# Kernel tuning notes

Hardware: AMD Instinct MI355X
Metric: run time of the kernel (lower is better)

Reference implementation:

```python
import jax, jax.numpy as jnp
import numpy as np
import math

N = 4096
E = 512          # hidden_dim
H = 8            # num_heads
MAX_STEPS = 100
D_TIME = E // 2  # 256
D_STAT = E // 4  # 128


def _time_encoding():
    # sinusoidal table [MAX_STEPS, D_TIME], matching the torch buffer
    pos = jnp.arange(MAX_STEPS, dtype=jnp.float32)[:, None]
    div = jnp.exp(jnp.arange(0, D_TIME, 2, dtype=jnp.float32) * (-math.log(10000.0) / D_TIME))
    ang = pos * div  # [MAX_STEPS, D_TIME//2]
    return jnp.stack([jnp.sin(ang), jnp.cos(ang)], axis=-1).reshape(MAX_STEPS, D_TIME)


def setup_inputs() -> dict:
    key = jax.random.key(0)
    ks = jax.random.split(key, 12)
    w = 0.02
    return {
        "x": jax.random.normal(ks[0], (N, E), jnp.float32),
        "derived_mask": jax.random.randint(ks[1], (N,), 0, 2, jnp.int32),
        "step_numbers": jax.random.randint(ks[2], (N,), 0, MAX_STEPS, jnp.int32),
        "status_embed": jax.random.normal(ks[3], (2, D_STAT), jnp.float32),
        "in_proj_w": jax.random.normal(ks[4], (3 * E, E), jnp.float32) * w,
        "in_proj_b": jnp.zeros((3 * E,), jnp.float32),
        "out_proj_w": jax.random.normal(ks[5], (E, E), jnp.float32) * w,
        "out_proj_b": jnp.zeros((E,), jnp.float32),
        "mlp_w": jax.random.normal(ks[6], (E, E + D_STAT + D_TIME), jnp.float32) * w,
        "mlp_b": jnp.zeros((E,), jnp.float32),
        "ln_gamma": jnp.ones((E,), jnp.float32),
        "ln_beta": jnp.zeros((E,), jnp.float32),
    }


def reference(x, derived_mask, step_numbers, status_embed, in_proj_w, in_proj_b,
              out_proj_w, out_proj_b, mlp_w, mlp_b, ln_gamma, ln_beta):
    n = x.shape[0]
    hd = E // H

    # --- multihead self-attention with dynamic step-based mask ---
    qkv = x @ in_proj_w.T + in_proj_b                      # [N, 3E]
    q, k, v = jnp.split(qkv, 3, axis=-1)
    q = q.reshape(n, H, hd).transpose(1, 0, 2)             # [H, N, hd]
    k = k.reshape(n, H, hd).transpose(1, 0, 2)
    v = v.reshape(n, H, hd).transpose(1, 0, 2)

    scores = jnp.einsum('hnd,hmd->hnm', q, k) / math.sqrt(hd)   # [H, N, N]
    # mask[i, j] = True  <=>  step[j] - step[i] < 0 (blocked, -inf)
    blocked = (step_numbers[None, :] - step_numbers[:, None]) < 0
    scores = jnp.where(blocked[None, :, :], jnp.float32(-1e9), scores)
    attn = jax.nn.softmax(scores, axis=-1)
    ctx = jnp.einsum('hnm,hmd->hnd', attn, v)              # [H, N, hd]
    ctx = ctx.transpose(1, 0, 2).reshape(n, E)
    x_att = ctx @ out_proj_w.T + out_proj_b                # [N, E]

    # --- embeddings ---
    status = status_embed[derived_mask]                    # [N, E/4]
    step_c = jnp.clip(step_numbers, 0, MAX_STEPS - 1)
    time_emb = _time_encoding()[step_c]                    # [N, E/2]

    # --- fused output MLP: Linear -> LayerNorm -> ReLU ---
    combined = jnp.concatenate([x_att, status, time_emb], axis=-1)  # [N, 7E/4]
    h = combined @ mlp_w.T + mlp_b                         # [N, E]
    mu = jnp.mean(h, axis=-1, keepdims=True)
    var = jnp.mean((h - mu) ** 2, axis=-1, keepdims=True)
    h = (h - mu) / jnp.sqrt(var + 1e-5) * ln_gamma + ln_beta
    out = jnp.maximum(h, 0.0)
    return x + out
```

## Files before the change

### kernel.cpp

```cpp
#include <hip/hip_runtime.h>
#include <hip/hip_bf16.h>
#include <math.h>

typedef __bf16 bf16x8 __attribute__((ext_vector_type(8)));
typedef __bf16 bf16x4 __attribute__((ext_vector_type(4)));
typedef float f32x4 __attribute__((ext_vector_type(4)));
typedef float f32x16 __attribute__((ext_vector_type(16)));

#define N_TOK 4096
#define EDIM 512
#define NHEAD 8
#define HD 64
#define LDCOMB 896
#define NBIN 100
#define SPLITK 4
#define BK 64
#define NQT 32

#define NU_CVT 3264
#define NU_TC 64
#define NU_ADD 128
#define NU_TMAT 128
#define NB_PREP (NU_CVT + NU_TC + NU_ADD + NU_TMAT + 1)

__device__ __forceinline__ unsigned int pk2(float a, float b) {
    union { __bf16 h[2]; unsigned int u; } x;
    x.h[0] = (__bf16)a; x.h[1] = (__bf16)b;
    return x.u;
}

__global__ __launch_bounds__(256) void prep_kernel(
    const float* __restrict__ x, const float* __restrict__ w_in,
    const float* __restrict__ w_mlp, const float* __restrict__ w_out,
    const float* __restrict__ status, const float* __restrict__ out_b,
    const float* __restrict__ mlp_b, const int* __restrict__ steps,
    __bf16* __restrict__ x_bf, __bf16* __restrict__ wqkv_bf,
    __bf16* __restrict__ wmlp_bf, __bf16* __restrict__ woutT_bf,
    float* __restrict__ add2, __bf16* __restrict__ tmat,
    int* __restrict__ perm, int* __restrict__ sstep,
    int* __restrict__ bs_row, int* __restrict__ qinfo) {
    __shared__ float T[64][65];
    __shared__ int hist[NBIN];
    __shared__ int offs[NBIN];
    const int bid = blockIdx.x;
    const int tid = threadIdx.x;
    const int wave = tid >> 6, lane = tid & 63;

    if (bid < NU_CVT) {
        int i = bid * 256 + tid;
        const int n0 = N_TOK * EDIM / 4;
        const int n1 = 3 * EDIM * EDIM / 4;
        const float* src; __bf16* dst;
        if (i < n0)           { src = x; dst = x_bf; }
        else if (i < n0 + n1) { i -= n0; src = w_in; dst = wqkv_bf; }
        else                  { i -= n0 + n1; src = w_mlp; dst = wmlp_bf; }
        const float4 v = ((const float4*)src)[i];
        bf16x4 o;
        o[0] = (__bf16)v.x; o[1] = (__bf16)v.y; o[2] = (__bf16)v.z; o[3] = (__bf16)v.w;
        ((bf16x4*)dst)[i] = o;
    } else if (bid < NU_CVT + NU_TC) {
        const int b2 = bid - NU_CVT;
        const int m0 = (b2 >> 3) * 64, k0 = (b2 & 7) * 64;
        const int row = tid >> 2, c4 = (tid & 3) * 16;
        #pragma unroll
        for (int i = 0; i < 4; i++) {
            const float4 v = *(const float4*)&w_out[(size_t)(m0 + row) * EDIM + k0 + c4 + i * 4];
            T[row][c4 + i * 4 + 0] = v.x;
            T[row][c4 + i * 4 + 1] = v.y;
            T[row][c4 + i * 4 + 2] = v.z;
            T[row][c4 + i * 4 + 3] = v.w;
        }
        __syncthreads();
        const int kr = tid >> 2, m16 = (tid & 3) * 16;
        bf16x8 o0, o1;
        #pragma unroll
        for (int i = 0; i < 8; i++) o0[i] = (__bf16)T[m16 + i][kr];
        #pragma unroll
        for (int i = 0; i < 8; i++) o1[i] = (__bf16)T[m16 + 8 + i][kr];
        *(bf16x8*)&woutT_bf[(size_t)(k0 + kr) * EDIM + m0 + m16] = o0;
        *(bf16x8*)&woutT_bf[(size_t)(k0 + kr) * EDIM + m0 + m16 + 8] = o1;
    } else if (bid < NU_CVT + NU_TC + NU_ADD) {
        const int j = (bid - NU_CVT - NU_TC) * 4 + wave;
        const float* wr = w_mlp + (size_t)j * LDCOMB;
        const int k8 = lane * 8;
        const float4 wa = *(const float4*)&wr[k8], wb = *(const float4*)&wr[k8 + 4];
        const float4 oa = *(const float4*)&out_b[k8], ob = *(const float4*)&out_b[k8 + 4];
        float b = wa.x * oa.x + wa.y * oa.y + wa.z * oa.z + wa.w * oa.w +
                  wb.x * ob.x + wb.y * ob.y + wb.z * ob.z + wb.w * ob.w;
        const int c2 = lane * 2;
        const float w0 = wr[EDIM + c2], w1 = wr[EDIM + c2 + 1];
        float s0 = status[c2] * w0 + status[c2 + 1] * w1;
        float s1 = status[128 + c2] * w0 + status[129 + c2] * w1;
        #pragma unroll
        for (int m = 1; m < 64; m <<= 1) {
            b += __shfl_xor(b, m);
            s0 += __shfl_xor(s0, m);
            s1 += __shfl_xor(s1, m);
        }
        if (lane == 0) {
            const float bb = b + mlp_b[j];
            add2[j] = s0 + bb;
            add2[EDIM + j] = s1 + bb;
        }
    } else if (bid < NU_CVT + NU_TC + NU_ADD + NU_TMAT) {
        const int st = bid - NU_CVT - NU_TC - NU_ADD;
        const int c = tid;
        const int pp = c >> 1;
        const float div = expf((float)(2 * pp) * (-9.210340371976184f / 256.0f));
        const float ang = (float)st * div;
        tmat[st * 256 + c] = (__bf16)((c & 1) ? cosf(ang) : sinf(ang));
    } else {
        if (tid < NBIN) hist[tid] = 0;
        __syncthreads();
        for (int i = tid; i < N_TOK; i += 256)
            atomicAdd(&hist[min(max(steps[i], 0), NBIN - 1)], 1);
        __syncthreads();
        if (tid == 0) {
            int acc = 0;
            for (int s = 0; s < NBIN; s++) { offs[s] = acc; acc += hist[s]; }
        }
        __syncthreads();
        if (tid < NBIN) hist[tid] = offs[tid];
        __syncthreads();
        for (int i = tid; i < N_TOK; i += 256) {
            const int s = min(max(steps[i], 0), NBIN - 1);
            const int pos = atomicAdd(&offs[s], 1);
            perm[pos] = i;
            sstep[pos] = s;
        }
        __syncthreads();
        for (int q = tid; q < N_TOK; q += 256)
            bs_row[q] = hist[sstep[q]];
        __syncthreads();
        for (int qt = tid; qt < NQT; qt += 256) {
            qinfo[qt * 2] = bs_row[qt * 128] & ~(BK - 1);
            qinfo[qt * 2 + 1] = bs_row[qt * 128 + 127];
        }
    }
}

__global__ __launch_bounds__(256) void gemm2_kernel(const __bf16* __restrict__ x_bf,
                                                    const __bf16* __restrict__ wqkv_bf,
                                                    const float* __restrict__ b_in,
                                                    const int* __restrict__ perm,
                                                    __bf16* __restrict__ qs,
                                                    __bf16* __restrict__ ks,
                                                    __bf16* __restrict__ vt,
                                                    const __bf16* __restrict__ wmlp_bf,
                                                    const __bf16* __restrict__ woutT_bf,
                                                    __bf16* __restrict__ weff_bf,
                                                    const __bf16* __restrict__ tmat,
                                                    float* __restrict__ tv) {
    __shared__ __attribute__((aligned(16))) union {
        struct { __bf16 As[128][40]; __bf16 Bs[128][40]; } g;
        __bf16 T[128][72];
    } sm;
    __shared__ int pr[128];
    const int bid = blockIdx.x;
    const int tid = threadIdx.x;
    const int wave = tid >> 6, lane = tid & 63;
    const int wm = (wave >> 1) * 64, wn = (wave & 1) * 64;
    const int lr = lane & 15, lq = lane >> 4;

    const __bf16 *A, *B;
    int lda, ldb, bm, bn, K, mode;
    if (bid < 384) {
        A = x_bf; lda = EDIM; B = wqkv_bf; ldb = EDIM; K = EDIM; mode = 0;
        bm = (bid & 31) * 128; bn = (bid >> 5) * 128;
        if (tid < 128) pr[tid] = perm[bm + tid];
    } else if (bid < 400) {
        const int b2 = bid - 384;
        A = wmlp_bf; lda = LDCOMB; B = woutT_bf; ldb = EDIM; K = EDIM; mode = 1;
        bm = (b2 & 3) * 128; bn = (b2 >> 2) * 128;
    } else {
        const int b3 = bid - 400;
        A = tmat; lda = 256; B = wmlp_bf + 640; ldb = LDCOMB; K = 256; mode = 2;
        bm = 0; bn = b3 * 128;
    }

    f32x4 acc[4][4] = {};
    for (int k0 = 0; k0 < K; k0 += 32) {
        __syncthreads();
        #pragma unroll
        for (int c = tid; c < 512; c += 256) {
            const int row = c >> 2, k8 = (c & 3) * 8;
            const int arow = (mode == 0) ? pr[row] : (bm + row);
            *(bf16x8*)&sm.g.As[row][k8] = *(const bf16x8*)&A[(size_t)arow * lda + k0 + k8];
            *(bf16x8*)&sm.g.Bs[row][k8] = *(const bf16x8*)&B[(size_t)(bn + row) * ldb + k0 + k8];
        }
        __syncthreads();
        bf16x8 af[4], bfr[4];
        #pragma unroll
        for (int i = 0; i < 4; i++) {
            af[i]  = *(const bf16x8*)&sm.g.As[wm + i * 16 + lr][lq * 8];
            bfr[i] = *(const bf16x8*)&sm.g.Bs[wn + i * 16 + lr][lq * 8];
        }
        #pragma unroll
        for (int i = 0; i < 4; i++)
            #pragma unroll
            for (int j = 0; j < 4; j++)
                acc[i][j] = __builtin_amdgcn_mfma_f32_16x16x32_bf16(af[i], bfr[j], acc[i][j], 0, 0, 0);
    }

    if (mode == 1) {
        #pragma unroll
        for (int i = 0; i < 4; i++)
            #pragma unroll
            for (int j = 0; j < 4; j++) {
                const int col = bn + wn + j * 16 + lr;
                #pragma unroll
                for (int r = 0; r < 4; r++)
                    weff_bf[(size_t)(bm + wm + i * 16 + lq * 4 + r) * EDIM + col] =
                        (__bf16)acc[i][j][r];
            }
    } else if (mode == 2) {
        #pragma unroll
        for (int i = 0; i < 4; i++)
            #pragma unroll
            for (int j = 0; j < 4; j++) {
                const int col = bn + wn + j * 16 + lr;
                #pragma unroll
                for (int r = 0; r < 4; r++) {
                    const int row = wm + i * 16 + lq * 4 + r;
                    if (row < NBIN) tv[(size_t)row * EDIM + col] = acc[i][j][r];
                }
            }
    } else if (bn < 512) {
        const float SC = 0.125f * 1.44269504f;
        #pragma unroll
        for (int i = 0; i < 4; i++)
            #pragma unroll
            for (int j = 0; j < 4; j++) {
                const int col = bn + wn + j * 16 + lr;
                const float bv = b_in[col];
                #pragma unroll
                for (int r = 0; r < 4; r++)
                    qs[(size_t)(bm + wm + i * 16 + lq * 4 + r) * EDIM + col] =
                        (__bf16)((acc[i][j][r] + bv) * SC);
            }
    } else if (bn < 1024) {
        #pragma unroll
        for (int i = 0; i < 4; i++)
            #pragma unroll
            for (int j = 0; j < 4; j++) {
                const int col = bn + wn + j * 16 + lr;
                const float bv = b_in[col];
                #pragma unroll
                for (int r = 0; r < 4; r++)
                    ks[(size_t)(bm + wm + i * 16 + lq * 4 + r) * EDIM + (col - 512)] =
                        (__bf16)(acc[i][j][r] + bv);
            }
    } else {
        #pragma unroll
        for (int half = 0; half < 2; half++) {
            __syncthreads();
            if ((wave & 1) == half) {
                #pragma unroll
                for (int i = 0; i < 4; i++)
                    #pragma unroll
                    for (int j = 0; j < 4; j++) {
                        const float bv = b_in[bn + wn + j * 16 + lr];
                        #pragma unroll
                        for (int r = 0; r < 4; r++)
                            sm.T[wm + i * 16 + lq * 4 + r][j * 16 + lr] =
                                (__bf16)(acc[i][j][r] + bv);
                    }
            }
            __syncthreads();
            for (int u = tid; u < 1024; u += 256) {
                const int d = u & 63, t8 = (u >> 6) * 8;
                bf16x8 v;
                #pragma unroll
                for (int j = 0; j < 8; j++) v[j] = sm.T[t8 + j][d];
                const int dim = (bn - 1024) + half * 64 + d;
                *(bf16x8*)&vt[(size_t)dim * N_TOK + bm + t8] = v;
            }
        }
    }
}

__global__ __launch_bounds__(256, 4) void attn_kernel(const __bf16* __restrict__ qs,
                                                      const __bf16* __restrict__ ks,
                                                      const __bf16* __restrict__ vt,
                                                      const int* __restrict__ bs_row,
                                                      const int* __restrict__ qinfo,
                                                      __bf16* __restrict__ po,
                                                      float* __restrict__ pl) {
    __shared__ __attribute__((aligned(16))) __bf16 KVs[2][2][4160];

    const int h = blockIdx.x & 7;
    const int qtile = blockIdx.x >> 3;
    const int ck = blockIdx.y;
    const int tid = threadIdx.x, wave = tid >> 6, lane = tid & 63;
    const int l31 = lane & 31, hi = lane >> 5;
    const int wq0 = qtile * 128 + wave * 32;

    const int kt0 = qinfo[qtile * 2];
    const int bs_blockmax = qinfo[qtile * 2 + 1];
    const int nt = (N_TOK - kt0) / BK;
    const int kta = kt0 + ((nt * ck) / SPLITK) * BK;
    const int ktb = kt0 + ((nt * (ck + 1)) / SPLITK) * BK;

    bf16x8 aq[4];
    {
        const __bf16* qrow = qs + (size_t)(wq0 + l31) * EDIM + h * HD;
        #pragma unroll
        for (int m = 0; m < 4; m++) aq[m] = *(const bf16x8*)&qrow[m * 16 + hi * 8];
    }
    const int bsq = bs_row[wq0 + l31];

    bf16x8 ones;
    #pragma unroll
    for (int i = 0; i < 8; i++) ones[i] = (__bf16)1.0f;

    f32x16 lacc = {};
    f32x16 o0 = {}, o1 = {};

    const int ro = lane >> 3;
    const int sc = (lane & 7) ^ ro;

    auto stage = [&](int buf, int kt_s) {
        #pragma unroll
        for (int i = 0; i < 2; i++) {
            const int g = wave * 2 + i;
            const __bf16* gk = ks + (size_t)(kt_s + g * 8 + ro) * EDIM + h * HD + sc * 8;
            __builtin_amdgcn_global_load_lds(
                (const __attribute__((address_space(1))) unsigned int*)gk,
                (__attribute__((address_space(3))) unsigned int*)&KVs[buf][0][g * 520],
                16, 0, 0);
            const __bf16* gv = vt + (size_t)(h * HD + g * 8 + ro) * N_TOK + kt_s + sc * 8;
            __builtin_amdgcn_global_load_lds(
                (const __attribute__((address_space(1))) unsigned int*)gv,
                (__attribute__((address_space(3))) unsigned int*)&KVs[buf][1][g * 520],
                16, 0, 0);
        }
    };

    #define LDOFF(r, c) (((r) >> 3) * 520 + ((r) & 7) * 64 + ((((c) ^ ((r) & 7))) << 3))

    if (kta < ktb) stage(0, kta);
    __syncthreads();

    int cur = 0;
    for (int kt = kta; kt < ktb; kt += BK) {
        if (kt + BK < ktb) stage(cur ^ 1, kt + BK);
        const __bf16* Kl = &KVs[cur][0][0];
        const __bf16* Vl = &KVs[cur][1][0];

        __builtin_amdgcn_s_setprio(1);
        #pragma unroll
        for (int t = 0; t < 2; t++) {
            f32x16 s = {};
            #pragma unroll
            for (int m = 0; m < 4; m++) {
                const bf16x8 kb = *(const bf16x8*)&Kl[LDOFF(t * 32 + l31, 2 * m + hi)];
                s = __builtin_amdgcn_mfma_f32_32x32x16_bf16(kb, aq[m], s, 0, 0, 0);
            }
            if (kt < bs_blockmax) {
                const int tokb = kt + t * 32 + 4 * hi;
                #pragma unroll
                for (int r = 0; r < 16; r++) {
                    const int tok = tokb + (r & 3) + 8 * (r >> 2);
                    if (tok < bsq) s[r] = -1e9f;
                }
            }
            unsigned int pk[8];
            #pragma unroll
            for (int m = 0; m < 8; m++)
                pk[m] = pk2(exp2f(s[2 * m]), exp2f(s[2 * m + 1]));
            asm("v_permlane32_swap_b32 %0, %1" : "+v"(pk[0]), "+v"(pk[2]));
            asm("v_permlane32_swap_b32 %0, %1" : "+v"(pk[1]), "+v"(pk[3]));
            asm("v_permlane32_swap_b32 %0, %1" : "+v"(pk[4]), "+v"(pk[6]));
            asm("v_permlane32_swap_b32 %0, %1" : "+v"(pk[5]), "+v"(pk[7]));
            union { unsigned int u[4]; bf16x8 v; } f0, f1;
            f0.u[0] = pk[0]; f0.u[1] = pk[1]; f0.u[2] = pk[2]; f0.u[3] = pk[3];
            f1.u[0] = pk[4]; f1.u[1] = pk[5]; f1.u[2] = pk[6]; f1.u[3] = pk[7];
            lacc = __builtin_amdgcn_mfma_f32_32x32x16_bf16(ones, f0.v, lacc, 0, 0, 0);
            lacc = __builtin_amdgcn_mfma_f32_32x32x16_bf16(ones, f1.v, lacc, 0, 0, 0);
            #pragma unroll
            for (int h2 = 0; h2 < 2; h2++) {
                const bf16x8 va = *(const bf16x8*)&Vl[LDOFF(l31, 4 * t + 2 * h2 + hi)];
                const bf16x8 vb = *(const bf16x8*)&Vl[LDOFF(32 + l31, 4 * t + 2 * h2 + hi)];
                const bf16x8 pf = h2 ? f1.v : f0.v;
                o0 = __builtin_amdgcn_mfma_f32_32x32x16_bf16(va, pf, o0, 0, 0, 0);
                o1 = __builtin_amdgcn_mfma_f32_32x32x16_bf16(vb, pf, o1, 0, 0, 0);
            }
        }
        __builtin_amdgcn_s_setprio(0);
        __syncthreads();
        cur ^= 1;
    }
    #undef LDOFF

    __bf16* pob = po + (((size_t)(ck * NHEAD + h) * N_TOK) + wq0 + l31) * HD;
    #pragma unroll
    for (int rg = 0; rg < 4; rg++) {
        bf16x4 ova, ovb;
        #pragma unroll
        for (int r = 0; r < 4; r++) { ova[r] = (__bf16)o0[rg * 4 + r]; ovb[r] = (__bf16)o1[rg * 4 + r]; }
        *(bf16x4*)&pob[rg * 8 + 4 * hi] = ova;
        *(bf16x4*)&pob[32 + rg * 8 + 4 * hi] = ovb;
    }
    if (hi == 0)
        pl[(size_t)(ck * NHEAD + h) * N_TOK + wq0 + l31] = lacc[0];
}

__global__ __launch_bounds__(256) void combine_kernel(const __bf16* __restrict__ po,
                                                      const float* __restrict__ pl,
                                                      const int* __restrict__ perm,
                                                      __bf16* __restrict__ ctx) {
    const int e = blockIdx.x * 256 + threadIdx.x;
    const int q = e >> 7;
    const int col = (e & 127) * 4;
    const int h = col >> 6, d = col & 63;
    float s0 = 0.f, s1 = 0.f, s2 = 0.f, s3 = 0.f, l = 0.f;
    #pragma unroll
    for (int c = 0; c < SPLITK; c++) {
        const bf16x4 v = *(const bf16x4*)&po[(((size_t)(c * NHEAD + h) * N_TOK) + q) * HD + d];
        s0 += (float)v[0]; s1 += (float)v[1]; s2 += (float)v[2]; s3 += (float)v[3];
        l += pl[(size_t)(c * NHEAD + h) * N_TOK + q];
    }
    const float rl = 1.0f / l;
    bf16x4 o;
    o[0] = (__bf16)(s0 * rl); o[1] = (__bf16)(s1 * rl);
    o[2] = (__bf16)(s2 * rl); o[3] = (__bf16)(s3 * rl);
    *(bf16x4*)&ctx[(size_t)perm[q] * EDIM + col] = o;
}

__global__ __launch_bounds__(256) void gemm_fused(const __bf16* __restrict__ A,
                                                  const __bf16* __restrict__ B,
                                                  const int* __restrict__ dmask,
                                                  const int* __restrict__ steps,
                                                  const float* __restrict__ add2,
                                                  const float* __restrict__ tv,
                                                  float* __restrict__ C) {
    __shared__ __attribute__((aligned(16))) __bf16 As[128][40];
    __shared__ __attribute__((aligned(16))) __bf16 Bs[128][40];
    const int tid = threadIdx.x;
    const int wave = tid >> 6, lane = tid & 63;
    const int wm = (wave >> 1) * 64, wn = (wave & 1) * 64;
    const int bm = blockIdx.x * 128, bn = blockIdx.y * 128;
    const int lr = lane & 15, lq = lane >> 4;

    f32x4 acc[4][4] = {};
    for (int k0 = 0; k0 < EDIM; k0 += 32) {
        __syncthreads();
        #pragma unroll
        for (int c = tid; c < 512; c += 256) {
            const int row = c >> 2, k8 = (c & 3) * 8;
            *(bf16x8*)&As[row][k8] = *(const bf16x8*)&A[(size_t)(bm + row) * EDIM + k0 + k8];
            *(bf16x8*)&Bs[row][k8] = *(const bf16x8*)&B[(size_t)(bn + row) * EDIM + k0 + k8];
        }
        __syncthreads();
        bf16x8 af[4], bfr[4];
        #pragma unroll
        for (int i = 0; i < 4; i++) {
            af[i]  = *(const bf16x8*)&As[wm + i * 16 + lr][lq * 8];
            bfr[i] = *(const bf16x8*)&Bs[wn + i * 16 + lr][lq * 8];
        }
        #pragma unroll
        for (int i = 0; i < 4; i++)
            #pragma unroll
            for (int j = 0; j < 4; j++)
                acc[i][j] = __builtin_amdgcn_mfma_f32_16x16x32_bf16(af[i], bfr[j], acc[i][j], 0, 0, 0);
    }

    int dmr[4][4], str[4][4];
    #pragma unroll
    for (int i = 0; i < 4; i++)
        #pragma unroll
        for (int r = 0; r < 4; r++) {
            const int row = bm + wm + i * 16 + lq * 4 + r;
            dmr[i][r] = dmask[row];
            str[i][r] = min(max(steps[row], 0), NBIN - 1);
        }
    #pragma unroll
    for (int i = 0; i < 4; i++)
        #pragma unroll
        for (int j = 0; j < 4; j++) {
            const int col = bn + wn + j * 16 + lr;
            #pragma unroll
            for (int r = 0; r < 4; r++) {
                const int row = bm + wm + i * 16 + lq * 4 + r;
                C[(size_t)row * EDIM + col] = acc[i][j][r]
                    + add2[dmr[i][r] * EDIM + col] + tv[str[i][r] * EDIM + col];
            }
        }
}

__global__ __launch_bounds__(256) void ln_kernel(const float* __restrict__ h,
                                                 const float* __restrict__ x,
                                                 const float* __restrict__ gamma,
                                                 const float* __restrict__ beta,
                                                 float* __restrict__ out) {
    const int row = blockIdx.x * 4 + (threadIdx.x >> 6);
    const int lane = threadIdx.x & 63;
    const float* hr = h + (size_t)row * EDIM;
    float4 v0 = ((const float4*)hr)[lane];
    float4 v1 = ((const float4*)hr)[64 + lane];
    float sum = v0.x + v0.y + v0.z + v0.w + v1.x + v1.y + v1.z + v1.w;
    float sq = v0.x * v0.x + v0.y * v0.y + v0.z * v0.z + v0.w * v0.w +
               v1.x * v1.x + v1.y * v1.y + v1.z * v1.z + v1.w * v1.w;
    #pragma unroll
    for (int m = 1; m < 64; m <<= 1) {
        sum += __shfl_xor(sum, m);
        sq  += __shfl_xor(sq, m);
    }
    const float mean = sum * (1.0f / EDIM);
    const float var = sq * (1.0f / EDIM) - mean * mean;
    const float rstd = rsqrtf(var + 1e-5f);
    const float* xr = x + (size_t)row * EDIM;
    float* orow = out + (size_t)row * EDIM;
    #pragma unroll
    for (int half = 0; half < 2; half++) {
        const float4 v = half ? v1 : v0;
        const int cb = half * 256 + lane * 4;
        const float* vp = (const float*)&v;
        float4 res;
        float tmp[4];
        #pragma unroll
        for (int i = 0; i < 4; i++) {
            const int c = cb + i;
            float t = (vp[i] - mean) * rstd * gamma[c] + beta[c];
            t = fmaxf(t, 0.f);
            tmp[i] = xr[c] + t;
        }
        res.x = tmp[0]; res.y = tmp[1]; res.z = tmp[2]; res.w = tmp[3];
        ((float4*)orow)[cb >> 2] = res;
    }
}

extern "C" void kernel_launch(void* const* d_in, const int* in_sizes, int n_in,
                              void* d_out, int out_size, void* d_ws, size_t ws_size,
                              hipStream_t stream) {
    const float* x      = (const float*)d_in[0];
    const int*   dmask  = (const int*)d_in[1];
    const int*   steps  = (const int*)d_in[2];
    const float* status = (const float*)d_in[3];
    const float* w_in   = (const float*)d_in[4];
    const float* b_in   = (const float*)d_in[5];
    const float* w_out  = (const float*)d_in[6];
    const float* b_out  = (const float*)d_in[7];
    const float* w_mlp  = (const float*)d_in[8];
    const float* b_mlp  = (const float*)d_in[9];
    const float* gamma  = (const float*)d_in[10];
    const float* beta   = (const float*)d_in[11];
    float* out = (float*)d_out;

    char* ws = (char*)d_ws;
    size_t off = 0;
    auto alloc = [&](size_t bytes) {
        void* ptr = ws + off;
        off = (off + bytes + 255) & ~(size_t)255;
        return ptr;
    };
    __bf16* x_bf    = (__bf16*)alloc((size_t)N_TOK * EDIM * 2);
    __bf16* wqkv_bf = (__bf16*)alloc((size_t)3 * EDIM * EDIM * 2);
    __bf16* wmlp_bf = (__bf16*)alloc((size_t)EDIM * LDCOMB * 2);
    __bf16* woutT_bf= (__bf16*)alloc((size_t)EDIM * EDIM * 2);
    __bf16* weff_bf = (__bf16*)alloc((size_t)EDIM * EDIM * 2);
    __bf16* qs_bf   = (__bf16*)alloc((size_t)N_TOK * EDIM * 2);
    __bf16* ks_bf   = (__bf16*)alloc((size_t)N_TOK * EDIM * 2);
    __bf16* vt_bf   = (__bf16*)alloc((size_t)EDIM * N_TOK * 2);
    __bf16* ctx_bf  = (__bf16*)alloc((size_t)N_TOK * EDIM * 2);
    float*  h_f32   = (float*)alloc((size_t)N_TOK * EDIM * 4);
    int*    perm    = (int*)alloc(N_TOK * 4);
    int*    sstep   = (int*)alloc(N_TOK * 4);
    int*    bs_row  = (int*)alloc(N_TOK * 4);
    int*    qinfo   = (int*)alloc(128 * 4);
    __bf16* po      = (__bf16*)alloc((size_t)SPLITK * NHEAD * N_TOK * HD * 2);
    float*  pl      = (float*)alloc((size_t)SPLITK * NHEAD * N_TOK * 4);
    float*  add2    = (float*)alloc(2 * EDIM * 4);
    float*  tv      = (float*)alloc((size_t)NBIN * EDIM * 4);
    __bf16* tmat    = (__bf16*)alloc(128 * 256 * 2);

    prep_kernel<<<NB_PREP, 256, 0, stream>>>(
        x, w_in, w_mlp, w_out, status, b_out, b_mlp, steps,
        x_bf, wqkv_bf, wmlp_bf, woutT_bf, add2, tmat, perm, sstep, bs_row, qinfo);
    gemm2_kernel<<<404, 256, 0, stream>>>(
        x_bf, wqkv_bf, b_in, perm, qs_bf, ks_bf, vt_bf,
        wmlp_bf, woutT_bf, weff_bf, tmat, tv);
    attn_kernel<<<dim3(NQT * NHEAD, SPLITK), 256, 0, stream>>>(
        qs_bf, ks_bf, vt_bf, bs_row, qinfo, po, pl);
    combine_kernel<<<(N_TOK * EDIM) / 1024, 256, 0, stream>>>(po, pl, perm, ctx_bf);
    gemm_fused<<<dim3(N_TOK / 128, EDIM / 128), 256, 0, stream>>>(
        ctx_bf, weff_bf, dmask, steps, add2, tv, h_f32);
    ln_kernel<<<N_TOK / 4, 256, 0, stream>>>(h_f32, x, gamma, beta, out);
}
```

Measured before the change: 198.9 us.

## Make attention waves independent with register-prefetched K/V and finer query tiles

New measurement: 251.5 us. 26.4% more time.

```diff
diff --git a/kernel.cpp b/kernel.cpp
--- a/kernel.cpp
+++ b/kernel.cpp
@@ -13,9 +13,9 @@
 #define HD 64
 #define LDCOMB 896
 #define NBIN 100
-#define SPLITK 4
+#define SPLITK 8
 #define BK 64
-#define NQT 32
+#define NQT 128
 
 #define NU_CVT 3264
 #define NU_TC 64
@@ -133,8 +133,8 @@
             bs_row[q] = hist[sstep[q]];
         __syncthreads();
         for (int qt = tid; qt < NQT; qt += 256) {
-            qinfo[qt * 2] = bs_row[qt * 128] & ~(BK - 1);
-            qinfo[qt * 2 + 1] = bs_row[qt * 128 + 127];
+            qinfo[qt * 2] = bs_row[qt * 32] & ~(BK - 1);
+            qinfo[qt * 2 + 1] = bs_row[qt * 32 + 31];
         }
     }
 }
@@ -279,24 +279,24 @@
     }
 }
 
-__global__ __launch_bounds__(256, 4) void attn_kernel(const __bf16* __restrict__ qs,
+__global__ __launch_bounds__(256, 2) void attn_kernel(const __bf16* __restrict__ qs,
                                                       const __bf16* __restrict__ ks,
                                                       const __bf16* __restrict__ vt,
                                                       const int* __restrict__ bs_row,
                                                       const int* __restrict__ qinfo,
                                                       __bf16* __restrict__ po,
                                                       float* __restrict__ pl) {
-    __shared__ __attribute__((aligned(16))) __bf16 KVs[2][2][4160];
-
-    const int h = blockIdx.x & 7;
-    const int qtile = blockIdx.x >> 3;
-    const int ck = blockIdx.y;
+    const int bid = blockIdx.x;
+    const int h = bid & 7;
     const int tid = threadIdx.x, wave = tid >> 6, lane = tid & 63;
     const int l31 = lane & 31, hi = lane >> 5;
-    const int wq0 = qtile * 128 + wave * 32;
-
-    const int kt0 = qinfo[qtile * 2];
-    const int bs_blockmax = qinfo[qtile * 2 + 1];
+    const int slot = (bid >> 3) * 4 + wave;
+    const int qt = slot & (NQT - 1);
+    const int ck = slot >> 7;
+    const int wq0 = qt * 32;
+
+    const int kt0 = qinfo[qt * 2];
+    const int bs_max = qinfo[qt * 2 + 1];
     const int nt = (N_TOK - kt0) / BK;
     const int kta = kt0 + ((nt * ck) / SPLITK) * BK;
     const int ktb = kt0 + ((nt * (ck + 1)) / SPLITK) * BK;
@@ -316,47 +316,36 @@
     f32x16 lacc = {};
     f32x16 o0 = {}, o1 = {};
 
-    const int ro = lane >> 3;
-    const int sc = (lane & 7) ^ ro;
-
-    auto stage = [&](int buf, int kt_s) {
-        #pragma unroll
-        for (int i = 0; i < 2; i++) {
-            const int g = wave * 2 + i;
-            const __bf16* gk = ks + (size_t)(kt_s + g * 8 + ro) * EDIM + h * HD + sc * 8;
-            __builtin_amdgcn_global_load_lds(
-                (const __attribute__((address_space(1))) unsigned int*)gk,
-                (__attribute__((address_space(3))) unsigned int*)&KVs[buf][0][g * 520],
-                16, 0, 0);
-            const __bf16* gv = vt + (size_t)(h * HD + g * 8 + ro) * N_TOK + kt_s + sc * 8;
-            __builtin_amdgcn_global_load_lds(
-                (const __attribute__((address_space(1))) unsigned int*)gv,
-                (__attribute__((address_space(3))) unsigned int*)&KVs[buf][1][g * 520],
-                16, 0, 0);
+    const __bf16* kbase = ks + (size_t)l31 * EDIM + h * HD + hi * 8;
+    const __bf16* vbase = vt + (size_t)(h * HD + l31) * N_TOK + hi * 8;
+
+    auto loadK = [&](bf16x8 (&kf)[8], int kt) {
+        const __bf16* p0 = kbase + (size_t)kt * EDIM;
+        const __bf16* p1 = p0 + 32 * EDIM;
+        #pragma unroll
+        for (int m = 0; m < 4; m++) {
+            kf[m]     = *(const bf16x8*)&p0[m * 16];
+            kf[4 + m] = *(const bf16x8*)&p1[m * 16];
         }
     };
-
-    #define LDOFF(r, c) (((r) >> 3) * 520 + ((r) & 7) * 64 + ((((c) ^ ((r) & 7))) << 3))
-
-    if (kta < ktb) stage(0, kta);
-    __syncthreads();
-
-    int cur = 0;
-    for (int kt = kta; kt < ktb; kt += BK) {
-        if (kt + BK < ktb) stage(cur ^ 1, kt + BK);
-        const __bf16* Kl = &KVs[cur][0][0];
-        const __bf16* Vl = &KVs[cur][1][0];
-
-        __builtin_amdgcn_s_setprio(1);
+    auto loadV = [&](bf16x8 (&vf)[8], int kt) {
+        const __bf16* p0 = vbase + kt;
+        const __bf16* p1 = p0 + (size_t)32 * N_TOK;
+        #pragma unroll
+        for (int j = 0; j < 4; j++) {
+            vf[j]     = *(const bf16x8*)&p0[j * 16];
+            vf[4 + j] = *(const bf16x8*)&p1[j * 16];
+        }
+    };
+
+    auto compute = [&](const bf16x8 (&kf)[8], const bf16x8 (&vf)[8], int kt) {
         #pragma unroll
         for (int t = 0; t < 2; t++) {
             f32x16 s = {};
             #pragma unroll
-            for (int m = 0; m < 4; m++) {
-                const bf16x8 kb = *(const bf16x8*)&Kl[LDOFF(t * 32 + l31, 2 * m + hi)];
-                s = __builtin_amdgcn_mfma_f32_32x32x16_bf16(kb, aq[m], s, 0, 0, 0);
-            }
-            if (kt < bs_blockmax) {
+            for (int m = 0; m < 4; m++)
+                s = __builtin_amdgcn_mfma_f32_32x32x16_bf16(kf[t * 4 + m], aq[m], s, 0, 0, 0);
+            if (kt < bs_max) {
                 const int tokb = kt + t * 32 + 4 * hi;
                 #pragma unroll
                 for (int r = 0; r < 16; r++) {
@@ -379,18 +368,22 @@
             lacc = __builtin_amdgcn_mfma_f32_32x32x16_bf16(ones, f1.v, lacc, 0, 0, 0);
             #pragma unroll
             for (int h2 = 0; h2 < 2; h2++) {
-                const bf16x8 va = *(const bf16x8*)&Vl[LDOFF(l31, 4 * t + 2 * h2 + hi)];
-                const bf16x8 vb = *(const bf16x8*)&Vl[LDOFF(32 + l31, 4 * t + 2 * h2 + hi)];
                 const bf16x8 pf = h2 ? f1.v : f0.v;
-                o0 = __builtin_amdgcn_mfma_f32_32x32x16_bf16(va, pf, o0, 0, 0, 0);
-                o1 = __builtin_amdgcn_mfma_f32_32x32x16_bf16(vb, pf, o1, 0, 0, 0);
-            }
-        }
-        __builtin_amdgcn_s_setprio(0);
-        __syncthreads();
-        cur ^= 1;
-    }
-    #undef LDOFF
+                o0 = __builtin_amdgcn_mfma_f32_32x32x16_bf16(vf[t * 2 + h2], pf, o0, 0, 0, 0);
+                o1 = __builtin_amdgcn_mfma_f32_32x32x16_bf16(vf[4 + t * 2 + h2], pf, o1, 0, 0, 0);
+            }
+        }
+    };
+
+    bf16x8 kfA[8], vfA[8], kfB[8], vfB[8];
+    if (kta < ktb) { loadK(kfA, kta); loadV(vfA, kta); }
+    for (int kt = kta; kt < ktb; kt += 2 * BK) {
+        if (kt + BK < ktb) { loadK(kfB, kt + BK); loadV(vfB, kt + BK); }
+        compute(kfA, vfA, kt);
+        if (kt + BK >= ktb) break;
+        if (kt + 2 * BK < ktb) { loadK(kfA, kt + 2 * BK); loadV(vfA, kt + 2 * BK); }
+        compute(kfB, vfB, kt + BK);
+    }
 
     __bf16* pob = po + (((size_t)(ck * NHEAD + h) * N_TOK) + wq0 + l31) * HD;
     #pragma unroll
@@ -567,7 +560,7 @@
     int*    perm    = (int*)alloc(N_TOK * 4);
     int*    sstep   = (int*)alloc(N_TOK * 4);
     int*    bs_row  = (int*)alloc(N_TOK * 4);
-    int*    qinfo   = (int*)alloc(128 * 4);
+    int*    qinfo   = (int*)alloc(2 * NQT * 4);
     __bf16* po      = (__bf16*)alloc((size_t)SPLITK * NHEAD * N_TOK * HD * 2);
     float*  pl      = (float*)alloc((size_t)SPLITK * NHEAD * N_TOK * 4);
     float*  add2    = (float*)alloc(2 * EDIM * 4);
@@ -580,7 +573,7 @@
     gemm2_kernel<<<404, 256, 0, stream>>>(
         x_bf, wqkv_bf, b_in, perm, qs_bf, ks_bf, vt_bf,
         wmlp_bf, woutT_bf, weff_bf, tmat, tv);
-    attn_kernel<<<dim3(NQT * NHEAD, SPLITK), 256, 0, stream>>>(
+    attn_kernel<<<dim3(NQT * NHEAD * SPLITK / 4), 256, 0, stream>>>(
         qs_bf, ks_bf, vt_bf, bs_row, qinfo, po, pl);
     combine_kernel<<<(N_TOK * EDIM) / 1024, 256, 0, stream>>>(po, pl, perm, ctx_bf);
     gemm_fused<<<dim3(N_TOK / 128, EDIM / 128), 256, 0, stream>>>(
```
